# Kernel tuning notes

Measured on AMD Instinct MI355X. Metric: run time of the kernel, lower is better.

## Reference

```python
import jax, jax.numpy as jnp
import numpy as np

D = 256
NODE_COUNTS = [200000, 50000, 12000, 4000]  # n_src per block; dst of block l = NODE_COUNTS[l+1]
EDGE_COUNTS = [500000, 120000, 40000]


def setup_inputs() -> dict:
    key = jax.random.key(0)
    ks = jax.random.split(key, 16)
    x = jax.random.normal(ks[0], (NODE_COUNTS[0], D), dtype=jnp.float32)
    inp = {"x": x}
    scale = 1.0 / np.sqrt(D)
    ki = 1
    for l in range(3):
        inp[f"Wself{l}"] = jax.random.normal(ks[ki], (D, D), dtype=jnp.float32) * scale; ki += 1
        inp[f"Wneigh{l}"] = jax.random.normal(ks[ki], (D, D), dtype=jnp.float32) * scale; ki += 1
        inp[f"b{l}"] = jnp.zeros((D,), dtype=jnp.float32)
    for l in range(3):
        e = EDGE_COUNTS[l]
        inp[f"src{l}"] = jax.random.randint(ks[ki], (e,), 0, NODE_COUNTS[l]); ki += 1
        inp[f"dst{l}"] = jax.random.randint(ks[ki], (e,), 0, NODE_COUNTS[l + 1]); ki += 1
    inp["nd0"], inp["nd1"], inp["nd2"] = NODE_COUNTS[1], NODE_COUNTS[2], NODE_COUNTS[3]
    return inp


def _sage_layer(h, src, dst, n_dst, Ws, Wn, b, relu=True):
    # DGL SAGEConv('mean'): out = fc_self(h_dst) + fc_neigh(mean_{u in N(v)} h_u) + bias
    h_dst = h[:n_dst]
    msgs = h[src]                                               # [E, d] gather
    agg = jax.ops.segment_sum(msgs, dst, num_segments=n_dst)    # [n_dst, d]
    deg = jax.ops.segment_sum(jnp.ones((dst.shape[0],), h.dtype), dst, num_segments=n_dst)
    mean = agg / jnp.maximum(deg, 1.0)[:, None]
    out = h_dst @ Ws + mean @ Wn + b
    return jax.nn.relu(out) if relu else out


def reference(x, Wself0, Wneigh0, b0, Wself1, Wneigh1, b1, Wself2, Wneigh2, b2,
              src0, dst0, src1, dst1, src2, dst2, nd0, nd1, nd2):
    h = _sage_layer(x, src0, dst0, nd0, Wself0, Wneigh0, b0)
    h = _sage_layer(h, src1, dst1, nd1, Wself1, Wneigh1, b1)
    h = _sage_layer(h, src2, dst2, nd2, Wself2, Wneigh2, b2)
    return h
```

## Files before the change

### kernel.cpp

```cpp
#include <hip/hip_runtime.h>
#include <stdint.h>

#define D 256

typedef __attribute__((ext_vector_type(8))) short bf16x8;
typedef __attribute__((ext_vector_type(4))) float f32x4;

__device__ inline unsigned short f2bf(float f) {
    union { float f; uint32_t u; } v; v.f = f;
    return (unsigned short)((v.u + 0x7FFFu + ((v.u >> 16) & 1u)) >> 16);
}
__device__ inline float bf2f(unsigned short b) {
    return __uint_as_float(((uint32_t)b) << 16);
}

#define SEG0 0
#define SEG1 50176
#define SEG2 62464
#define CURTOT 66560
#define NBLK 65

#define WBLK 1536
#define XBLK 6250

struct PreArgs {
    const float* w[6];
    const float* x;
    unsigned short* wt;
    unsigned short* xb;
    const int* d0; const int* d1; const int* d2;
    int* cur;
    int E0, E01, Etot, cblk0;
};

__global__ __launch_bounds__(256) void fused_pre(PreArgs a)
{
    int b = blockIdx.x;
    if (b < WBLK) {
        int t = b * 256 + threadIdx.x;
        int m = t >> 16, e = t & 65535;
        int col = e >> 8, k = e & 255;
        a.wt[t] = f2bf(a.w[m][(k << 8) + col]);
    } else if (b < WBLK + XBLK) {
        long t = (long)(b - WBLK) * 256 + threadIdx.x;
        const float4* p = (const float4*)a.x + t * 2;
        float4 v0 = p[0], v1 = p[1];
        unsigned short r[8] = {f2bf(v0.x), f2bf(v0.y), f2bf(v0.z), f2bf(v0.w),
                               f2bf(v1.x), f2bf(v1.y), f2bf(v1.z), f2bf(v1.w)};
        *(uint4*)(a.xb + t * 8) = *(uint4*)r;
    } else {
        int e = (b - a.cblk0) * 256 + threadIdx.x;
        if (e >= a.Etot) return;
        int base, d;
        if (e < a.E0)       { base = SEG0; d = a.d0[e]; }
        else if (e < a.E01) { base = SEG1; d = a.d1[e - a.E0]; }
        else                { base = SEG2; d = a.d2[e - a.E01]; }
        atomicAdd(&a.cur[base + d], 1);
    }
}

__global__ __launch_bounds__(256) void scan_blocks(
    int* __restrict__ cur, int* __restrict__ bsum)
{
    __shared__ int wsum[4];
    int tid = threadIdx.x, lane = tid & 63, wid = tid >> 6;
    int base = blockIdx.x * 1024 + tid * 4;
    int4 v = *(int4*)(cur + base);
    int t0 = v.x, t01 = t0 + v.y, t012 = t01 + v.z, tot = t012 + v.w;
    int incl = tot;
    #pragma unroll
    for (int ofs = 1; ofs < 64; ofs <<= 1) {
        int t = __shfl_up(incl, ofs, 64);
        if (lane >= ofs) incl += t;
    }
    if (lane == 63) wsum[wid] = incl;
    __syncthreads();
    if (tid == 0) {
        int run = 0;
        #pragma unroll
        for (int w = 0; w < 4; ++w) { int t = wsum[w]; wsum[w] = run; run += t; }
        bsum[blockIdx.x] = run;
    }
    __syncthreads();
    int texcl = wsum[wid] + incl - tot;
    v.x = texcl; v.y = texcl + t0; v.z = texcl + t01; v.w = texcl + t012;
    *(int4*)(cur + base) = v;
}

__global__ __launch_bounds__(128) void scan_bsums(
    const int* __restrict__ bsum, int* __restrict__ bscan)
{
    __shared__ int s[NBLK];
    int tid = threadIdx.x;
    if (tid < NBLK) s[tid] = bsum[tid];
    __syncthreads();
    if (tid == 0) {
        int run = 0;
        for (int b = 0; b < 49; ++b)  { int t = s[b]; s[b] = run; run += t; }
        run = 0;
        for (int b = 49; b < 61; ++b) { int t = s[b]; s[b] = run; run += t; }
        run = 0;
        for (int b = 61; b < 65; ++b) { int t = s[b]; s[b] = run; run += t; }
    }
    __syncthreads();
    if (tid < NBLK) bscan[tid] = s[tid];
}

__global__ __launch_bounds__(256) void scan_addback(
    int* __restrict__ cur, const int* __restrict__ bscan)
{
    int base = blockIdx.x * 1024 + threadIdx.x * 4;
    int add = bscan[blockIdx.x];
    int4 v = *(int4*)(cur + base);
    v.x += add; v.y += add; v.z += add; v.w += add;
    *(int4*)(cur + base) = v;
}

__global__ __launch_bounds__(256) void fill_all(
    const int* __restrict__ s0, const int* __restrict__ s1, const int* __restrict__ s2,
    const int* __restrict__ d0, const int* __restrict__ d1, const int* __restrict__ d2,
    int* __restrict__ cur, int* __restrict__ idx, int E0, int E01, int Etot)
{
    int e = blockIdx.x * 256 + threadIdx.x;
    if (e >= Etot) return;
    int base, d, s, ib;
    if (e < E0)       { base = SEG0; d = d0[e];       s = s0[e];       ib = 0; }
    else if (e < E01) { base = SEG1; d = d1[e - E0];  s = s1[e - E0];  ib = E0; }
    else              { base = SEG2; d = d2[e - E01]; s = s2[e - E01]; ib = E01; }
    int p = atomicAdd(&cur[base + d], 1);
    idx[ib + p] = s;
}

template<int BF16IN>
__global__ __launch_bounds__(256) void gather_mean_k(
    const void* __restrict__ hv, const int* __restrict__ idx,
    const int* __restrict__ curseg, unsigned short* __restrict__ mean, int M)
{
    int t = blockIdx.x * blockDim.x + threadIdx.x;
    int w = t >> 6, lane = t & 63;
    if (w >= M) return;
    int e0 = w ? curseg[w - 1] : 0;
    int e1 = curseg[w];
    float4 acc0 = make_float4(0.f, 0.f, 0.f, 0.f);
    float4 acc1 = make_float4(0.f, 0.f, 0.f, 0.f);
    int e = e0;
    if (BF16IN) {
        const unsigned short* h = (const unsigned short*)hv;
        for (; e + 3 < e1; e += 4) {
            int sa = idx[e], sb = idx[e + 1], sc = idx[e + 2], sd = idx[e + 3];
            ushort4 va = *(const ushort4*)(h + (size_t)sa * D + lane * 4);
            ushort4 vb = *(const ushort4*)(h + (size_t)sb * D + lane * 4);
            ushort4 vc = *(const ushort4*)(h + (size_t)sc * D + lane * 4);
            ushort4 vd = *(const ushort4*)(h + (size_t)sd * D + lane * 4);
            acc0.x += bf2f(va.x) + bf2f(vb.x);
            acc0.y += bf2f(va.y) + bf2f(vb.y);
            acc0.z += bf2f(va.z) + bf2f(vb.z);
            acc0.w += bf2f(va.w) + bf2f(vb.w);
            acc1.x += bf2f(vc.x) + bf2f(vd.x);
            acc1.y += bf2f(vc.y) + bf2f(vd.y);
            acc1.z += bf2f(vc.z) + bf2f(vd.z);
            acc1.w += bf2f(vc.w) + bf2f(vd.w);
        }
        for (; e < e1; ++e) {
            int sa = idx[e];
            ushort4 va = *(const ushort4*)(h + (size_t)sa * D + lane * 4);
            acc0.x += bf2f(va.x); acc0.y += bf2f(va.y);
            acc0.z += bf2f(va.z); acc0.w += bf2f(va.w);
        }
    } else {
        const float* h = (const float*)hv;
        for (; e + 3 < e1; e += 4) {
            int sa = idx[e], sb = idx[e + 1], sc = idx[e + 2], sd = idx[e + 3];
            float4 va = *((const float4*)(h + (size_t)sa * D) + lane);
            float4 vb = *((const float4*)(h + (size_t)sb * D) + lane);
            float4 vc = *((const float4*)(h + (size_t)sc * D) + lane);
            float4 vd = *((const float4*)(h + (size_t)sd * D) + lane);
            acc0.x += va.x + vb.x; acc0.y += va.y + vb.y;
            acc0.z += va.z + vb.z; acc0.w += va.w + vb.w;
            acc1.x += vc.x + vd.x; acc1.y += vc.y + vd.y;
            acc1.z += vc.z + vd.z; acc1.w += vc.w + vd.w;
        }
        for (; e < e1; ++e) {
            int sa = idx[e];
            float4 va = *((const float4*)(h + (size_t)sa * D) + lane);
            acc0.x += va.x; acc0.y += va.y; acc0.z += va.z; acc0.w += va.w;
        }
    }
    acc0.x += acc1.x; acc0.y += acc1.y; acc0.z += acc1.z; acc0.w += acc1.w;
    float r = 1.0f / fmaxf((float)(e1 - e0), 1.0f);
    ushort4 o;
    o.x = f2bf(acc0.x * r); o.y = f2bf(acc0.y * r);
    o.z = f2bf(acc0.z * r); o.w = f2bf(acc0.w * r);
    *(ushort4*)(mean + (size_t)w * D + lane * 4) = o;
}

template<int FINAL>
__global__ __launch_bounds__(256, 2) void sage_gemm_mfma(
    const unsigned short* __restrict__ A1,
    const unsigned short* __restrict__ A2,
    const unsigned short* __restrict__ Wt1,
    const unsigned short* __restrict__ Wt2,
    const float* __restrict__ bias,
    void* __restrict__ outv,
    int M)
{
    __shared__ unsigned short As[128 * 32];
    __shared__ unsigned short Bs[256 * 32];

    int tid = threadIdx.x;
    int lane = tid & 63, wid = tid >> 6;
    int wr = wid >> 1, wc = wid & 1;
    int m0 = blockIdx.x * 128;
    int l15 = lane & 15, lq = lane >> 4;

    f32x4 acc[4][8] = {};

    for (int kt = 0; kt < 16; ++kt) {
        const unsigned short* A = (kt < 8) ? A1 : A2;
        const unsigned short* B = (kt < 8) ? Wt1 : Wt2;
        int kk = (kt & 7) * 32;
        #pragma unroll
        for (int q = 0; q < 2; ++q) {
            int ch = q * 256 + tid;
            int r = ch >> 2, c16 = ch & 3;
            int gr = m0 + r; if (gr >= M) gr = M - 1;
            const unsigned short* src = A + (size_t)gr * 256 + kk + c16 * 8;
            __builtin_amdgcn_global_load_lds(
                (const __attribute__((address_space(1))) void*)src,
                (__attribute__((address_space(3))) void*)(As + (q * 256 + wid * 64) * 8),
                16, 0, 0);
        }
        #pragma unroll
        for (int q = 0; q < 4; ++q) {
            int ch = q * 256 + tid;
            int col = ch >> 2, c16 = ch & 3;
            const unsigned short* src = B + (size_t)col * 256 + kk + c16 * 8;
            __builtin_amdgcn_global_load_lds(
                (const __attribute__((address_space(1))) void*)src,
                (__attribute__((address_space(3))) void*)(Bs + (q * 256 + wid * 64) * 8),
                16, 0, 0);
        }
        __syncthreads();

        bf16x8 af[4], bfr[8];
        #pragma unroll
        for (int i = 0; i < 4; ++i)
            af[i] = *(const bf16x8*)(As + (wr * 64 + i * 16 + l15) * 32 + lq * 8);
        #pragma unroll
        for (int i = 0; i < 8; ++i)
            bfr[i] = *(const bf16x8*)(Bs + (wc * 128 + i * 16 + l15) * 32 + lq * 8);

        #pragma unroll
        for (int mr = 0; mr < 4; ++mr)
            #pragma unroll
            for (int nc = 0; nc < 8; ++nc)
                acc[mr][nc] = __builtin_amdgcn_mfma_f32_16x16x32_bf16(
                    af[mr], bfr[nc], acc[mr][nc], 0, 0, 0);
        __syncthreads();
    }

    #pragma unroll
    for (int nc = 0; nc < 8; ++nc) {
        int gc = wc * 128 + nc * 16 + l15;
        float bv = bias[gc];
        #pragma unroll
        for (int mr = 0; mr < 4; ++mr) {
            #pragma unroll
            for (int reg = 0; reg < 4; ++reg) {
                int gr = m0 + wr * 64 + mr * 16 + lq * 4 + reg;
                if (gr < M) {
                    float v = fmaxf(acc[mr][nc][reg] + bv, 0.f);
                    if (FINAL) ((float*)outv)[(size_t)gr * 256 + gc] = v;
                    else ((unsigned short*)outv)[(size_t)gr * 256 + gc] = f2bf(v);
                }
            }
        }
    }
}

extern "C" void kernel_launch(void* const* d_in, const int* in_sizes, int n_in,
                              void* d_out, int out_size, void* d_ws, size_t ws_size,
                              hipStream_t stream) {
    const float* x = (const float*)d_in[0];
    const float* Wself[3]  = {(const float*)d_in[1], (const float*)d_in[4], (const float*)d_in[7]};
    const float* Wneigh[3] = {(const float*)d_in[2], (const float*)d_in[5], (const float*)d_in[8]};
    const float* bias[3]   = {(const float*)d_in[3], (const float*)d_in[6], (const float*)d_in[9]};
    const int* src[3] = {(const int*)d_in[10], (const int*)d_in[12], (const int*)d_in[14]};
    const int* dst[3] = {(const int*)d_in[11], (const int*)d_in[13], (const int*)d_in[15]};
    int E[3]    = {in_sizes[10], in_sizes[12], in_sizes[14]};
    int ndst[3] = {50000, 12000, 4000};
    int E0 = E[0], E01 = E[0] + E[1], Etot = E[0] + E[1] + E[2];

    unsigned short* xb    = (unsigned short*)d_ws;
    unsigned short* h1b   = xb + (size_t)50000 * D;
    unsigned short* h2b   = h1b + (size_t)50000 * D;
    unsigned short* meanb = h2b + (size_t)12000 * D;
    unsigned short* wt    = meanb + (size_t)50000 * D;
    int* cur   = (int*)(wt + 6 * 65536);
    int* bsum  = cur + CURTOT;
    int* bscan = bsum + 80;
    int* idxa  = bscan + 80;

    hipMemsetAsync(cur, 0, CURTOT * sizeof(int), stream);

    PreArgs pa;
    pa.w[0] = Wself[0]; pa.w[1] = Wneigh[0];
    pa.w[2] = Wself[1]; pa.w[3] = Wneigh[1];
    pa.w[4] = Wself[2]; pa.w[5] = Wneigh[2];
    pa.x = x; pa.wt = wt; pa.xb = xb;
    pa.d0 = dst[0]; pa.d1 = dst[1]; pa.d2 = dst[2];
    pa.cur = cur; pa.E0 = E0; pa.E01 = E01; pa.Etot = Etot;
    pa.cblk0 = WBLK + XBLK;
    int cblk = (Etot + 255) / 256;
    fused_pre<<<WBLK + XBLK + cblk, 256, 0, stream>>>(pa);

    scan_blocks<<<NBLK, 256, 0, stream>>>(cur, bsum);
    scan_bsums<<<1, 128, 0, stream>>>(bsum, bscan);
    scan_addback<<<NBLK, 256, 0, stream>>>(cur, bscan);
    fill_all<<<(Etot + 255) / 256, 256, 0, stream>>>(src[0], src[1], src[2],
        dst[0], dst[1], dst[2], cur, idxa, E0, E01, Etot);

    const unsigned short* hin_b[3] = {xb, h1b, h2b};
    void* houts[3] = {h1b, h2b, d_out};
    int segb[3] = {SEG0, SEG1, SEG2};
    int idxb[3] = {0, E0, E01};

    for (int l = 0; l < 3; ++l) {
        int M = ndst[l];
        int gt = M * 64;
        if (l == 0)
            gather_mean_k<0><<<(gt + 255) / 256, 256, 0, stream>>>(
                x, idxa + idxb[l], cur + segb[l], meanb, M);
        else
            gather_mean_k<1><<<(gt + 255) / 256, 256, 0, stream>>>(
                hin_b[l], idxa + idxb[l], cur + segb[l], meanb, M);

        dim3 grid((M + 127) / 128);
        if (l < 2)
            sage_gemm_mfma<0><<<grid, 256, 0, stream>>>(hin_b[l], meanb,
                wt + (size_t)(2 * l) * 65536, wt + (size_t)(2 * l + 1) * 65536,
                bias[l], houts[l], M);
        else
            sage_gemm_mfma<1><<<grid, 256, 0, stream>>>(hin_b[l], meanb,
                wt + (size_t)(2 * l) * 65536, wt + (size_t)(2 * l + 1) * 65536,
                bias[l], houts[l], M);
    }
}
```

Measured before the change: 290.2 us.

## Fuse x bf16 conversion into layer-0 GEMM and split GEMM N across blocks

The separate pass that converted the first 50000 rows of x to bf16 is removed from the preprocessing kernel. The layer-0 GEMM now reads fp32 x directly, converts it in registers and stores it to LDS, which saves a full write and re-read of a bf16 copy. The GEMM tile is also reduced from 128x256 to 128x128, with a second grid dimension over N, to double the block count and lower register pressure. The cost is that A tiles are loaded twice, once per N-half, and the fp32 path uses ordinary loads instead of direct global-to-LDS loads.

```diff
diff --git a/kernel.cpp b/kernel.cpp
--- a/kernel.cpp
+++ b/kernel.cpp
@@ -21,16 +21,13 @@
 #define NBLK 65
 
 #define WBLK 1536
-#define XBLK 6250
 
 struct PreArgs {
     const float* w[6];
-    const float* x;
     unsigned short* wt;
-    unsigned short* xb;
     const int* d0; const int* d1; const int* d2;
     int* cur;
-    int E0, E01, Etot, cblk0;
+    int E0, E01, Etot;
 };
 
 __global__ __launch_bounds__(256) void fused_pre(PreArgs a)
@@ -41,15 +38,8 @@
         int m = t >> 16, e = t & 65535;
         int col = e >> 8, k = e & 255;
         a.wt[t] = f2bf(a.w[m][(k << 8) + col]);
-    } else if (b < WBLK + XBLK) {
-        long t = (long)(b - WBLK) * 256 + threadIdx.x;
-        const float4* p = (const float4*)a.x + t * 2;
-        float4 v0 = p[0], v1 = p[1];
-        unsigned short r[8] = {f2bf(v0.x), f2bf(v0.y), f2bf(v0.z), f2bf(v0.w),
-                               f2bf(v1.x), f2bf(v1.y), f2bf(v1.z), f2bf(v1.w)};
-        *(uint4*)(a.xb + t * 8) = *(uint4*)r;
     } else {
-        int e = (b - a.cblk0) * 256 + threadIdx.x;
+        int e = (b - WBLK) * 256 + threadIdx.x;
         if (e >= a.Etot) return;
         int base, d;
         if (e < a.E0)       { base = SEG0; d = a.d0[e]; }
@@ -194,9 +184,9 @@
     *(ushort4*)(mean + (size_t)w * D + lane * 4) = o;
 }
 
-template<int FINAL>
-__global__ __launch_bounds__(256, 2) void sage_gemm_mfma(
-    const unsigned short* __restrict__ A1,
+template<int FINAL, int A1F32>
+__global__ __launch_bounds__(256) void sage_gemm_mfma(
+    const void* __restrict__ A1v,
     const unsigned short* __restrict__ A2,
     const unsigned short* __restrict__ Wt1,
     const unsigned short* __restrict__ Wt2,
@@ -205,63 +195,79 @@
     int M)
 {
     __shared__ unsigned short As[128 * 32];
-    __shared__ unsigned short Bs[256 * 32];
+    __shared__ unsigned short Bs[128 * 32];
 
     int tid = threadIdx.x;
     int lane = tid & 63, wid = tid >> 6;
     int wr = wid >> 1, wc = wid & 1;
-    int m0 = blockIdx.x * 128;
+    int m0 = blockIdx.x * 128, n0 = blockIdx.y * 128;
     int l15 = lane & 15, lq = lane >> 4;
 
-    f32x4 acc[4][8] = {};
+    f32x4 acc[4][4] = {};
 
     for (int kt = 0; kt < 16; ++kt) {
-        const unsigned short* A = (kt < 8) ? A1 : A2;
-        const unsigned short* B = (kt < 8) ? Wt1 : Wt2;
         int kk = (kt & 7) * 32;
+        if (A1F32 && kt < 8) {
+            const float* A = (const float*)A1v;
+            #pragma unroll
+            for (int q = 0; q < 2; ++q) {
+                int ch = q * 256 + tid;
+                int r = ch >> 2, c16 = ch & 3;
+                int gr = m0 + r; if (gr >= M) gr = M - 1;
+                const float* s = A + (size_t)gr * 256 + kk + c16 * 8;
+                float4 u0 = *(const float4*)s;
+                float4 u1 = *(const float4*)(s + 4);
+                unsigned short rr[8] = {f2bf(u0.x), f2bf(u0.y), f2bf(u0.z), f2bf(u0.w),
+                                        f2bf(u1.x), f2bf(u1.y), f2bf(u1.z), f2bf(u1.w)};
+                *(uint4*)(As + ch * 8) = *(uint4*)rr;
+            }
+        } else {
+            const unsigned short* A = (kt < 8) ? (const unsigned short*)A1v : A2;
+            #pragma unroll
+            for (int q = 0; q < 2; ++q) {
+                int ch = q * 256 + tid;
+                int r = ch >> 2, c16 = ch & 3;
+                int gr = m0 + r; if (gr >= M) gr = M - 1;
+                const unsigned short* s = A + (size_t)gr * 256 + kk + c16 * 8;
+                __builtin_amdgcn_global_load_lds(
+                    (const __attribute__((address_space(1))) void*)s,
+                    (__attribute__((address_space(3))) void*)(As + (q * 256 + wid * 64) * 8),
+                    16, 0, 0);
+            }
+        }
+        {
+            const unsigned short* B = (kt < 8) ? Wt1 : Wt2;
+            #pragma unroll
+            for (int q = 0; q < 2; ++q) {
+                int ch = q * 256 + tid;
+                int col = ch >> 2, c16 = ch & 3;
+                const unsigned short* s = B + (size_t)(n0 + col) * 256 + kk + c16 * 8;
+                __builtin_amdgcn_global_load_lds(
+                    (const __attribute__((address_space(1))) void*)s,
+                    (__attribute__((address_space(3))) void*)(Bs + (q * 256 + wid * 64) * 8),
+                    16, 0, 0);
+            }
+        }
+        __syncthreads();
+
+        bf16x8 af[4], bfr[4];
         #pragma unroll
-        for (int q = 0; q < 2; ++q) {
-            int ch = q * 256 + tid;
-            int r = ch >> 2, c16 = ch & 3;
-            int gr = m0 + r; if (gr >= M) gr = M - 1;
-            const unsigned short* src = A + (size_t)gr * 256 + kk + c16 * 8;
-            __builtin_amdgcn_global_load_lds(
-                (const __attribute__((address_space(1))) void*)src,
-                (__attribute__((address_space(3))) void*)(As + (q * 256 + wid * 64) * 8),
-                16, 0, 0);
-        }
-        #pragma unroll
-        for (int q = 0; q < 4; ++q) {
-            int ch = q * 256 + tid;
-            int col = ch >> 2, c16 = ch & 3;
-            const unsigned short* src = B + (size_t)col * 256 + kk + c16 * 8;
-            __builtin_amdgcn_global_load_lds(
-                (const __attribute__((address_space(1))) void*)src,
-                (__attribute__((address_space(3))) void*)(Bs + (q * 256 + wid * 64) * 8),
-                16, 0, 0);
-        }
-        __syncthreads();
-
-        bf16x8 af[4], bfr[8];
-        #pragma unroll
-        for (int i = 0; i < 4; ++i)
-            af[i] = *(const bf16x8*)(As + (wr * 64 + i * 16 + l15) * 32 + lq * 8);
-        #pragma unroll
-        for (int i = 0; i < 8; ++i)
-            bfr[i] = *(const bf16x8*)(Bs + (wc * 128 + i * 16 + l15) * 32 + lq * 8);
-
+        for (int i = 0; i < 4; ++i) {
+            af[i]  = *(const bf16x8*)(As + (wr * 64 + i * 16 + l15) * 32 + lq * 8);
+            bfr[i] = *(const bf16x8*)(Bs + (wc * 64 + i * 16 + l15) * 32 + lq * 8);
+        }
         #pragma unroll
         for (int mr = 0; mr < 4; ++mr)
             #pragma unroll
-            for (int nc = 0; nc < 8; ++nc)
+            for (int nc = 0; nc < 4; ++nc)
                 acc[mr][nc] = __builtin_amdgcn_mfma_f32_16x16x32_bf16(
                     af[mr], bfr[nc], acc[mr][nc], 0, 0, 0);
         __syncthreads();
     }
 
     #pragma unroll
-    for (int nc = 0; nc < 8; ++nc) {
-        int gc = wc * 128 + nc * 16 + l15;
+    for (int nc = 0; nc < 4; ++nc) {
+        int gc = n0 + wc * 64 + nc * 16 + l15;
         float bv = bias[gc];
         #pragma unroll
         for (int mr = 0; mr < 4; ++mr) {
@@ -291,8 +297,7 @@
     int ndst[3] = {50000, 12000, 4000};
     int E0 = E[0], E01 = E[0] + E[1], Etot = E[0] + E[1] + E[2];
 
-    unsigned short* xb    = (unsigned short*)d_ws;
-    unsigned short* h1b   = xb + (size_t)50000 * D;
+    unsigned short* h1b   = (unsigned short*)d_ws;
     unsigned short* h2b   = h1b + (size_t)50000 * D;
     unsigned short* meanb = h2b + (size_t)12000 * D;
     unsigned short* wt    = meanb + (size_t)50000 * D;
@@ -307,12 +312,11 @@
     pa.w[0] = Wself[0]; pa.w[1] = Wneigh[0];
     pa.w[2] = Wself[1]; pa.w[3] = Wneigh[1];
     pa.w[4] = Wself[2]; pa.w[5] = Wneigh[2];
-    pa.x = x; pa.wt = wt; pa.xb = xb;
+    pa.wt = wt;
     pa.d0 = dst[0]; pa.d1 = dst[1]; pa.d2 = dst[2];
     pa.cur = cur; pa.E0 = E0; pa.E01 = E01; pa.Etot = Etot;
-    pa.cblk0 = WBLK + XBLK;
     int cblk = (Etot + 255) / 256;
-    fused_pre<<<WBLK + XBLK + cblk, 256, 0, stream>>>(pa);
+    fused_pre<<<WBLK + cblk, 256, 0, stream>>>(pa);
 
     scan_blocks<<<NBLK, 256, 0, stream>>>(cur, bsum);
     scan_bsums<<<1, 128, 0, stream>>>(bsum, bscan);
@@ -320,8 +324,6 @@
     fill_all<<<(Etot + 255) / 256, 256, 0, stream>>>(src[0], src[1], src[2],
         dst[0], dst[1], dst[2], cur, idxa, E0, E01, Etot);
 
-    const unsigned short* hin_b[3] = {xb, h1b, h2b};
-    void* houts[3] = {h1b, h2b, d_out};
     int segb[3] = {SEG0, SEG1, SEG2};
     int idxb[3] = {0, E0, E01};
 
@@ -333,16 +335,17 @@
                 x, idxa + idxb[l], cur + segb[l], meanb, M);
         else
             gather_mean_k<1><<<(gt + 255) / 256, 256, 0, stream>>>(
-                hin_b[l], idxa + idxb[l], cur + segb[l], meanb, M);
-
-        dim3 grid((M + 127) / 128);
-        if (l < 2)
-            sage_gemm_mfma<0><<<grid, 256, 0, stream>>>(hin_b[l], meanb,
-                wt + (size_t)(2 * l) * 65536, wt + (size_t)(2 * l + 1) * 65536,
-                bias[l], houts[l], M);
+                l == 1 ? h1b : h2b, idxa + idxb[l], cur + segb[l], meanb, M);
+
+        dim3 grid((M + 127) / 128, 2);
+        if (l == 0)
+            sage_gemm_mfma<0, 1><<<grid, 256, 0, stream>>>(x, meanb,
+                wt + 0 * 65536, wt + 1 * 65536, bias[0], h1b, M);
+        else if (l == 1)
+            sage_gemm_mfma<0, 0><<<grid, 256, 0, stream>>>(h1b, meanb,
+                wt + 2 * 65536, wt + 3 * 65536, bias[1], h2b, M);
         else
-            sage_gemm_mfma<1><<<grid, 256, 0, stream>>>(hin_b[l], meanb,
-                wt + (size_t)(2 * l) * 65536, wt + (size_t)(2 * l + 1) * 65536,
-                bias[l], houts[l], M);
-    }
-}
+            sage_gemm_mfma<1, 0><<<grid, 256, 0, stream>>>(h2b, meanb,
+                wt + 4 * 65536, wt + 5 * 65536, bias[2], d_out, M);
+    }
+}
```

New measurement: 270.9 us. 1.07x faster.
